# Performance work log

Measured on AMD Instinct MI355X. Metric: run time of the kernel, lower is better.

Reference implementation:

```python
import jax, jax.numpy as jnp
import numpy as np

D_MODEL = 1024
NUM_HEADS = 16
HEAD_DIM = D_MODEL // NUM_HEADS  # 64
ROPE_BASE = 10000.0


def _rope_tables(n_pos, dim):
    # 1D rotary tables for `dim` channels (rotate-half convention).
    inv_freq = 1.0 / (ROPE_BASE ** (jnp.arange(0, dim, 2, dtype=jnp.float32) / dim))
    ang = jnp.arange(n_pos, dtype=jnp.float32)[:, None] * inv_freq[None, :]  # (P, dim/2)
    cos = jnp.concatenate([jnp.cos(ang), jnp.cos(ang)], axis=-1)  # (P, dim)
    sin = jnp.concatenate([jnp.sin(ang), jnp.sin(ang)], axis=-1)
    return cos, sin


def _rotate_half(v):
    v1, v2 = jnp.split(v, 2, axis=-1)
    return jnp.concatenate([-v2, v1], axis=-1)


def rope_2d(x, H, W):
    # x: (N, H, W, nh, hd). First half of hd rotated by row index, second by col index.
    d_half = HEAD_DIM // 2
    x_h, x_w = x[..., :d_half], x[..., d_half:]
    cos_h, sin_h = _rope_tables(H, d_half)  # (H, d_half)
    cos_w, sin_w = _rope_tables(W, d_half)  # (W, d_half)
    cos_h = cos_h[None, :, None, None, :]
    sin_h = sin_h[None, :, None, None, :]
    cos_w = cos_w[None, None, :, None, :]
    sin_w = sin_w[None, None, :, None, :]
    x_h = x_h * cos_h + _rotate_half(x_h) * sin_h
    x_w = x_w * cos_w + _rotate_half(x_w) * sin_w
    return jnp.concatenate([x_h, x_w], axis=-1)


def setup_inputs() -> dict:
    key = jax.random.key(0)
    k_x, k_qkv, k_p, k_b = jax.random.split(key, 4)
    B, T, H, W = 4, 32, 16, 16
    x = jax.random.normal(k_x, (B, T, H, W, D_MODEL), dtype=jnp.float32)
    w_qkv = jax.random.normal(k_qkv, (D_MODEL, 3 * D_MODEL), dtype=jnp.float32) * 0.02
    w_proj = jax.random.normal(k_p, (D_MODEL, D_MODEL), dtype=jnp.float32) * 0.02
    b_proj = jax.random.normal(k_b, (D_MODEL,), dtype=jnp.float32) * 0.02
    return {"x": x, "w_qkv": w_qkv, "w_proj": w_proj, "b_proj": b_proj}


def reference(x, w_qkv, w_proj, b_proj):
    B, T, H, W, C = x.shape
    N, S = B * T, H * W
    scale = HEAD_DIM ** -0.5
    xf = x.reshape(N, S, C)
    qkv = xf @ w_qkv  # (N, S, 3C)  [qkv_bias=False]
    q, k, v = jnp.split(qkv, 3, axis=-1)
    q = q.reshape(N, H, W, NUM_HEADS, HEAD_DIM)
    k = k.reshape(N, H, W, NUM_HEADS, HEAD_DIM)
    v = v.reshape(N, S, NUM_HEADS, HEAD_DIM)
    q = rope_2d(q, H, W).reshape(N, S, NUM_HEADS, HEAD_DIM)
    k = rope_2d(k, H, W).reshape(N, S, NUM_HEADS, HEAD_DIM)
    attn = jnp.einsum('nshd,nthd->nhst', q, k) * scale  # (N, nh, S, S)
    attn = jax.nn.softmax(attn, axis=-1)  # attn_drop=0.0
    out = jnp.einsum('nhst,nthd->nshd', attn, v).reshape(N, S, C)
    out = out @ w_proj + b_proj
    return out.reshape(B, T, H, W, C)
```

## Files before the change

### kernel.cpp

```cpp
#include <hip/hip_runtime.h>
#include <hip/hip_bf16.h>
#include <stdint.h>

typedef __attribute__((ext_vector_type(8))) short bf16x8;
typedef __attribute__((ext_vector_type(4))) float f32x4;
typedef __attribute__((ext_vector_type(4))) unsigned short ushort4_t;

__device__ __forceinline__ unsigned short f2bf(float f) {
  union { float f; unsigned int i; } x; x.f = f;
  return (unsigned short)((x.i + 0x7fffu + ((x.i >> 16) & 1u)) >> 16);
}

__device__ __forceinline__ void gl_lds16(const void* g, void* l) {
  __builtin_amdgcn_global_load_lds(
      (const __attribute__((address_space(1))) unsigned int*)(uintptr_t)g,
      (__attribute__((address_space(3))) unsigned int*)(uint32_t)(uintptr_t)l,
      16, 0, 0);
}

__device__ __forceinline__ void bar() {
  asm volatile("" ::: "memory");
  __builtin_amdgcn_s_barrier();
  asm volatile("" ::: "memory");
}

__constant__ float INVF[16] = {
  1.0f,   0.56234132519f,  0.31622776601f,  0.17782794100f,
  0.1f,   0.056234132519f, 0.031622776601f, 0.017782794100f,
  0.01f,  0.0056234132519f,0.0031622776601f,0.0017782794100f,
  0.001f, 0.00056234132519f,0.00031622776601f,0.00017782794100f
};

__global__ __launch_bounds__(256) void k_conv_x(const float4* __restrict__ src,
                                                ushort4_t* __restrict__ dst, int n4) {
  int i = blockIdx.x * 256 + threadIdx.x;
  if (i < n4) {
    float4 v = src[i];
    ushort4_t r = { f2bf(v.x), f2bf(v.y), f2bf(v.z), f2bf(v.w) };
    dst[i] = r;
  }
}

__global__ __launch_bounds__(256) void k_transpose_bf16(const float* __restrict__ src,
                                                        unsigned short* __restrict__ dst,
                                                        int R, int C) {
  __shared__ unsigned short tile[64][65];
  const int bj = blockIdx.x, bi = blockIdx.y;
  const int t = threadIdx.x, lr = t >> 6, lc = t & 63;
  #pragma unroll
  for (int i = 0; i < 16; i++) {
    int r = i * 4 + lr;
    tile[r][lc] = f2bf(src[(size_t)(bi * 64 + r) * C + bj * 64 + lc]);
  }
  __syncthreads();
  #pragma unroll
  for (int i = 0; i < 16; i++) {
    int r = i * 4 + lr;
    dst[(size_t)(bj * 64 + r) * R + bi * 64 + lc] = tile[lc][r];
  }
}


#define LDA(dst, base, hm)                                                      \
  do {                                                                          \
    _Pragma("unroll") for (int t_ = 0; t_ < 4; t_++) {                          \
      dst[0][t_] = *(const bf16x8*)&base[(wm * 128 + (hm) * 64 + t_ * 16 + cl) * 64 + cf0]; \
      dst[1][t_] = *(const bf16x8*)&base[(wm * 128 + (hm) * 64 + t_ * 16 + cl) * 64 + cf1]; \
    }                                                                           \
  } while (0)

#define LDB(dst, base, hn)                                                      \
  do {                                                                          \
    _Pragma("unroll") for (int u_ = 0; u_ < 2; u_++) {                          \
      dst[0][u_] = *(const bf16x8*)&base[(wn * 64 + (hn) * 32 + u_ * 16 + cl) * 64 + cf0]; \
      dst[1][u_] = *(const bf16x8*)&base[(wn * 64 + (hn) * 32 + u_ * 16 + cl) * 64 + cf1]; \
    }                                                                           \
  } while (0)

#define MFMA_Q(hm, hn, AFR, BVR)                                                \
  do {                                                                          \
    __builtin_amdgcn_s_setprio(1);                                              \
    _Pragma("unroll") for (int kc_ = 0; kc_ < 2; kc_++)                         \
      _Pragma("unroll") for (int mt_ = 0; mt_ < 4; mt_++)                       \
        _Pragma("unroll") for (int u_ = 0; u_ < 2; u_++)                        \
          acc[(hm) * 4 + mt_][(hn) * 2 + u_] =                                  \
              __builtin_amdgcn_mfma_f32_16x16x32_bf16(                          \
                  AFR[kc_][mt_], BVR[kc_][u_],                                  \
                  acc[(hm) * 4 + mt_][(hn) * 2 + u_], 0, 0, 0);                 \
    __builtin_amdgcn_s_setprio(0);                                              \
  } while (0)

#define STAGE_A(tile_, half_)                                                   \
  do {                                                                          \
    const int so_ = ((tile_) & 1) * 16384;                                      \
    const int ko_ = (tile_) * 64;                                               \
    gl_lds16(aP[(half_) * 2] + ko_,     &As[so_ + ((half_) * 2) * 4096 + ldsW]);     \
    gl_lds16(aP[(half_) * 2 + 1] + ko_, &As[so_ + ((half_) * 2 + 1) * 4096 + ldsW]); \
  } while (0)

#define STAGE_B(tile_, half_)                                                   \
  do {                                                                          \
    const int so_ = ((tile_) & 1) * 16384;                                      \
    const int ko_ = (tile_) * 64;                                               \
    gl_lds16(bP[(half_) * 2] + ko_,     &Bs[so_ + ((half_) * 2) * 4096 + ldsW]);     \
    gl_lds16(bP[(half_) * 2 + 1] + ko_, &Bs[so_ + ((half_) * 2 + 1) * 4096 + ldsW]); \
  } while (0)

#define LGKM0() asm volatile("s_waitcnt lgkmcnt(0)" ::: "memory")
#define VMC(n)  asm volatile("s_waitcnt vmcnt(" #n ")" ::: "memory")

template<int F32OUT, int ROPE>
__global__ __launch_bounds__(512, 2) void k_gemm_bt(
    const unsigned short* __restrict__ A, const unsigned short* __restrict__ B,
    unsigned short* __restrict__ Cb, float* __restrict__ Cf,
    const float* __restrict__ bias, int M, int N, int K) {
  __shared__ __align__(16) unsigned short As[2 * 256 * 64];
  __shared__ __align__(16) unsigned short Bs[2 * 256 * 64];
  const int tid = threadIdx.x;
  const int lane = tid & 63, wid = tid >> 6;
  const int cl = lane & 15, gr = lane >> 4;
  const int wm = wid >> 2, wn = wid & 3;
  const int l8 = lane >> 3, l7 = lane & 7;

  const int gx = gridDim.x;
  const int nwg = gx * gridDim.y;
  const int fb = blockIdx.y * gx + blockIdx.x;
  const int q = nwg >> 3;
  const int nid = (fb & 7) * q + (fb >> 3);
  const int bx = nid % gx, by = nid / gx;
  const int mBase = by * 256, nBase = bx * 256;

  const int KT = K >> 6;
  const int ldsW = (wid * 8) * 64;
  const int cf0 = ((0 * 4 + gr) ^ (cl & 7)) * 8;
  const int cf1 = ((1 * 4 + gr) ^ (cl & 7)) * 8;

  const unsigned short* aP[4];
  const unsigned short* bP[4];
  #pragma unroll
  for (int i = 0; i < 4; i++) {
    aP[i] = A + (size_t)(mBase + i * 64 + wid * 8 + l8) * K + (l7 ^ l8) * 8;
    bP[i] = B + (size_t)(nBase + i * 64 + wid * 8 + l8) * K + (l7 ^ l8) * 8;
  }

  const f32x4 zero4 = {0.f, 0.f, 0.f, 0.f};
  f32x4 acc[8][4];
  #pragma unroll
  for (int a = 0; a < 8; a++)
    #pragma unroll
    for (int b = 0; b < 4; b++) acc[a][b] = zero4;

  STAGE_A(0, 0); STAGE_A(0, 1); STAGE_B(0, 0); STAGE_B(0, 1);
  STAGE_B(1, 0); STAGE_B(1, 1);
  VMC(4);
  bar();

  bf16x8 af[2][4], bva[2][2], bvb[2][2];

  for (int c = 0; c < KT; c += 2) {
    const unsigned short* a0 = As;
    const unsigned short* b0 = Bs;
    const unsigned short* a1 = As + 16384;
    const unsigned short* b1 = Bs + 16384;
    const int c2 = c + 2, c3 = c + 3;

    LDA(af, a0, 0); LDB(bva, b0, 0);
    STAGE_A(c + 1, 0);
    asm volatile("s_waitcnt lgkmcnt(8)" ::: "memory");
    bar(); LGKM0();
    MFMA_Q(0, 0, af, bva);
    bar();
    LDB(bvb, b0, 1);
    STAGE_A(c + 1, 1);
    bar(); LGKM0();
    MFMA_Q(0, 1, af, bvb);
    bar();
    LDA(af, a0, 1);
    if (c2 < KT) STAGE_B(c2, 0);
    bar(); LGKM0();
    MFMA_Q(1, 1, af, bvb);
    bar();
    if (c2 < KT) { STAGE_B(c2, 1); VMC(4); } else { VMC(0); }
    bar();
    MFMA_Q(1, 0, af, bva);
    bar();

    LDA(af, a1, 0); LDB(bva, b1, 0);
    if (c2 < KT) STAGE_A(c2, 0);
    asm volatile("s_waitcnt lgkmcnt(8)" ::: "memory");
    bar(); LGKM0();
    MFMA_Q(0, 0, af, bva);
    bar();
    LDB(bvb, b1, 1);
    if (c2 < KT) STAGE_A(c2, 1);
    bar(); LGKM0();
    MFMA_Q(0, 1, af, bvb);
    bar();
    LDA(af, a1, 1);
    if (c3 < KT) STAGE_B(c3, 0);
    bar(); LGKM0();
    MFMA_Q(1, 1, af, bvb);
    bar();
    if (c3 < KT)      { STAGE_B(c3, 1); VMC(4); }
    else if (c2 < KT) { VMC(0); }
    bar();
    MFMA_Q(1, 0, af, bva);
    if (c2 < KT) bar();
  }

  if (ROPE && nBase < 2048) {
    const float f2 = INVF[cl];
    #pragma unroll
    for (int amt = 0; amt < 8; amt++)
      #pragma unroll
      for (int r = 0; r < 4; r++) {
        const int sp = (mBase + wm * 128 + amt * 16 + gr * 4 + r) & 255;
        float sh, ch, sw, cw;
        __sincosf((float)(sp >> 4) * f2, &sh, &ch);
        __sincosf((float)(sp & 15) * f2, &sw, &cw);
        const float a = acc[amt][0][r], b = acc[amt][1][r];
        const float cc = acc[amt][2][r], d = acc[amt][3][r];
        acc[amt][0][r] = a * ch - b * sh;
        acc[amt][1][r] = b * ch + a * sh;
        acc[amt][2][r] = cc * cw - d * sw;
        acc[amt][3][r] = d * cw + cc * sw;
      }
  }

  #pragma unroll
  for (int amt = 0; amt < 8; amt++)
    #pragma unroll
    for (int nt = 0; nt < 4; nt++)
      #pragma unroll
      for (int r = 0; r < 4; r++) {
        const int row = mBase + wm * 128 + amt * 16 + gr * 4 + r;
        const int col = nBase + wn * 64 + nt * 16 + cl;
        const float v = acc[amt][nt][r];
        if (F32OUT) Cf[(size_t)row * N + col] = v + bias[col];
        else        Cb[(size_t)row * N + col] = f2bf(v);
      }
}

__global__ __launch_bounds__(256, 3) void k_attn(const unsigned short* __restrict__ qkv,
                                                 unsigned short* __restrict__ attn_out) {
  __shared__ __align__(16) unsigned short Qp[4][64 * 64];
  __shared__ __align__(16) unsigned short Kt[64 * 64];
  __shared__ __align__(16) unsigned short Vt[64 * 64];
  const int blk = blockIdx.x;
  const int n = blk >> 4, h = blk & 15;
  const int tid = threadIdx.x;
  const int lane = tid & 63, wid = tid >> 6;
  const int cl = lane & 15, gr = lane >> 4;
  const int l8 = lane >> 3, l7 = lane & 7;
  const unsigned short* qbase = qkv + (size_t)n * 256 * 3072 + h * 64;
  const unsigned short* kbase = qbase + 1024;
  const unsigned short* vbase = qbase + 2048;

  #pragma unroll
  for (int i = 0; i < 8; i++)
    gl_lds16(qbase + (size_t)(wid * 64 + i * 8 + l8) * 3072 + (l7 ^ l8) * 8,
             &Qp[wid][i * 8 * 64]);
  #pragma unroll
  for (int i = 0; i < 2; i++) {
    const int r0 = (wid * 2 + i) * 8;
    gl_lds16(kbase + (size_t)(r0 + l8) * 3072 + (l7 ^ l8) * 8, &Kt[r0 * 64]);
  }

  unsigned int vr[2][4];
  #pragma unroll
  for (int i = 0; i < 2; i++) {
    const int u = i * 256 + tid;
    const int t0 = u >> 5, d = (u & 31) * 2;
    #pragma unroll
    for (int k = 0; k < 4; k++)
      vr[i][k] = *(const unsigned int*)(vbase + (size_t)(t0 + 16 * k) * 3072 + d);
  }
  __syncthreads();

  bf16x8 qf[4][2];
  #pragma unroll
  for (int mt = 0; mt < 4; mt++)
    #pragma unroll
    for (int kc = 0; kc < 2; kc++)
      qf[mt][kc] = *(const bf16x8*)&Qp[wid][(mt * 16 + cl) * 64 + ((kc * 4 + gr) ^ (cl & 7)) * 8];

  const f32x4 zero4 = {0.f, 0.f, 0.f, 0.f};
  f32x4 o[4][4];
  float lsum[4][4];
  #pragma unroll
  for (int a = 0; a < 4; a++)
    #pragma unroll
    for (int b = 0; b < 4; b++) { o[a][b] = zero4; lsum[a][b] = 0.f; }

  for (int tc = 0; tc < 4; tc++) {
    #pragma unroll
    for (int i = 0; i < 2; i++) {
      const int u = i * 256 + tid;
      const int t0 = u >> 5, d = (u & 31) * 2;
      const unsigned int r0 = vr[i][0], r1 = vr[i][1], r2 = vr[i][2], r3 = vr[i][3];
      uint2 lo, hi;
      lo.x = (r0 & 0xffffu) | (r1 << 16);
      lo.y = (r2 & 0xffffu) | (r3 << 16);
      hi.x = (r0 >> 16) | (r1 & 0xffff0000u);
      hi.y = (r2 >> 16) | (r3 & 0xffff0000u);
      *(uint2*)&Vt[d * 64 + ((t0 >> 1) ^ (d & 7)) * 8 + (t0 & 1) * 4] = lo;
      const int d1 = d + 1;
      *(uint2*)&Vt[d1 * 64 + ((t0 >> 1) ^ (d1 & 7)) * 8 + (t0 & 1) * 4] = hi;
    }
    if (tc < 3) {
      #pragma unroll
      for (int i = 0; i < 2; i++) {
        const int u = i * 256 + tid;
        const int t0 = u >> 5, d = (u & 31) * 2;
        #pragma unroll
        for (int k = 0; k < 4; k++)
          vr[i][k] = *(const unsigned int*)(vbase + (size_t)((tc + 1) * 64 + t0 + 16 * k) * 3072 + d);
      }
    }

    #pragma unroll
    for (int mt = 0; mt < 4; mt++) {
      f32x4 sacc[4] = {zero4, zero4, zero4, zero4};
      #pragma unroll
      for (int kc = 0; kc < 2; kc++)
        #pragma unroll
        for (int nt = 0; nt < 4; nt++) {
          const bf16x8 kf = *(const bf16x8*)&Kt[(nt * 16 + cl) * 64 + ((kc * 4 + gr) ^ (cl & 7)) * 8];
          sacc[nt] = __builtin_amdgcn_mfma_f32_16x16x32_bf16(qf[mt][kc], kf, sacc[nt], 0, 0, 0);
        }
      #pragma unroll
      for (int r = 0; r < 4; r++) {
        const float p0 = __expf(sacc[0][r] * 0.125f);
        const float p1 = __expf(sacc[1][r] * 0.125f);
        const float p2 = __expf(sacc[2][r] * 0.125f);
        const float p3 = __expf(sacc[3][r] * 0.125f);
        lsum[mt][r] += (p0 + p1) + (p2 + p3);
        float2 f01; f01.x = p0; f01.y = p1;
        float2 f23; f23.x = p2; f23.y = p3;
        __hip_bfloat162 b01 = __float22bfloat162_rn(f01);
        __hip_bfloat162 b23 = __float22bfloat162_rn(f23);
        union { __hip_bfloat162 h; unsigned int u; } c0, c1;
        c0.h = b01; c1.h = b23;
        uint2 w; w.x = c0.u; w.y = c1.u;
        const int m = mt * 16 + gr * 4 + r;
        *(uint2*)&Qp[wid][m * 64 + ((cl >> 1) ^ (m & 7)) * 8 + (cl & 1) * 4] = w;
      }
    }
    __syncthreads();

    if (tc < 3) {
      #pragma unroll
      for (int i = 0; i < 2; i++) {
        const int r0 = (wid * 2 + i) * 8;
        gl_lds16(kbase + (size_t)((tc + 1) * 64 + r0 + l8) * 3072 + (l7 ^ l8) * 8, &Kt[r0 * 64]);
      }
    }

    #pragma unroll
    for (int kc = 0; kc < 2; kc++) {
      bf16x8 vf[4], pf[4];
      #pragma unroll
      for (int dt = 0; dt < 4; dt++)
        vf[dt] = *(const bf16x8*)&Vt[(dt * 16 + cl) * 64 + ((kc * 4 + gr) ^ (cl & 7)) * 8];
      #pragma unroll
      for (int mt = 0; mt < 4; mt++)
        pf[mt] = *(const bf16x8*)&Qp[wid][(mt * 16 + cl) * 64 + ((kc * 4 + gr) ^ (cl & 7)) * 8];
      #pragma unroll
      for (int mt = 0; mt < 4; mt++)
        #pragma unroll
        for (int dt = 0; dt < 4; dt++)
          o[mt][dt] = __builtin_amdgcn_mfma_f32_16x16x32_bf16(pf[mt], vf[dt], o[mt][dt], 0, 0, 0);
    }
    __syncthreads();
  }

  #pragma unroll
  for (int mt = 0; mt < 4; mt++)
    #pragma unroll
    for (int r = 0; r < 4; r++) {
      float l = lsum[mt][r];
      l += __shfl_xor(l, 1);
      l += __shfl_xor(l, 2);
      l += __shfl_xor(l, 4);
      l += __shfl_xor(l, 8);
      const float inv = 1.0f / l;
      const int srow = wid * 64 + mt * 16 + gr * 4 + r;
      #pragma unroll
      for (int dt = 0; dt < 4; dt++)
        attn_out[(size_t)(n * 256 + srow) * 1024 + h * 64 + dt * 16 + cl] =
            f2bf(o[mt][dt][r] * inv);
    }
}

extern "C" void kernel_launch(void* const* d_in, const int* in_sizes, int n_in,
                              void* d_out, int out_size, void* d_ws, size_t ws_size,
                              hipStream_t stream) {
  const float* x      = (const float*)d_in[0];
  const float* w_qkv  = (const float*)d_in[1];
  const float* w_proj = (const float*)d_in[2];
  const float* b_proj = (const float*)d_in[3];
  float* out = (float*)d_out;
  char* ws = (char*)d_ws;

  unsigned short* x_bf    = (unsigned short*)ws;
  unsigned short* wqkvT   = (unsigned short*)(ws + 67108864);
  unsigned short* wprojT  = (unsigned short*)(ws + 73400320);
  unsigned short* qkvb    = (unsigned short*)(ws + 75497472);
  unsigned short* attn_bf = x_bf;

  k_conv_x<<<32768, 256, 0, stream>>>((const float4*)x, (ushort4_t*)x_bf, 8388608);
  k_transpose_bf16<<<dim3(48, 16), 256, 0, stream>>>(w_qkv, wqkvT, 1024, 3072);
  k_transpose_bf16<<<dim3(16, 16), 256, 0, stream>>>(w_proj, wprojT, 1024, 1024);

  k_gemm_bt<0, 1><<<dim3(12, 128), 512, 0, stream>>>(x_bf, wqkvT, qkvb, nullptr, nullptr,
                                                     32768, 3072, 1024);
  k_attn<<<2048, 256, 0, stream>>>(qkvb, attn_bf);

  k_gemm_bt<1, 0><<<dim3(4, 128), 512, 0, stream>>>(attn_bf, wprojT, nullptr, out, b_proj,
                                                    32768, 1024, 1024);
}
```

Measured before the change: 640.8 us.

## Replace ping-pong barrier schedule with simple double-buffered K loop

Rewrites the GEMM main loop from a two-tile, barrier-heavy interleaved schedule into a single-tile-per-iteration double-buffered loop. All global-to-LDS loads for the next tile are issued up front, all LDS fragment reads are issued before the MFMAs with graded lgkmcnt waits, and a single vmcnt(0)+barrier closes each iteration. This removes many workgroup barriers and uses extra registers for a second A fragment set. The trade-off is a full vmcnt(0) stall at the end of each iteration, so global latency may be less hidden than before.

```diff
diff --git a/kernel.cpp b/kernel.cpp
--- a/kernel.cpp
+++ b/kernel.cpp
@@ -106,8 +106,7 @@
     gl_lds16(bP[(half_) * 2 + 1] + ko_, &Bs[so_ + ((half_) * 2 + 1) * 4096 + ldsW]); \
   } while (0)
 
-#define LGKM0() asm volatile("s_waitcnt lgkmcnt(0)" ::: "memory")
-#define VMC(n)  asm volatile("s_waitcnt vmcnt(" #n ")" ::: "memory")
+#define SBAR() __builtin_amdgcn_sched_barrier(0)
 
 template<int F32OUT, int ROPE>
 __global__ __launch_bounds__(512, 2) void k_gemm_bt(
@@ -151,61 +150,44 @@
     for (int b = 0; b < 4; b++) acc[a][b] = zero4;
 
   STAGE_A(0, 0); STAGE_A(0, 1); STAGE_B(0, 0); STAGE_B(0, 1);
-  STAGE_B(1, 0); STAGE_B(1, 1);
-  VMC(4);
+  asm volatile("s_waitcnt vmcnt(0)" ::: "memory");
   bar();
 
-  bf16x8 af[2][4], bva[2][2], bvb[2][2];
-
-  for (int c = 0; c < KT; c += 2) {
-    const unsigned short* a0 = As;
-    const unsigned short* b0 = Bs;
-    const unsigned short* a1 = As + 16384;
-    const unsigned short* b1 = Bs + 16384;
-    const int c2 = c + 2, c3 = c + 3;
-
-    LDA(af, a0, 0); LDB(bva, b0, 0);
-    STAGE_A(c + 1, 0);
+  bf16x8 af0[2][4], af1[2][4], bva[2][2], bvb[2][2];
+
+  for (int c = 0; c < KT; ++c) {
+    const int s = c & 1;
+    const unsigned short* as_ = As + s * 16384;
+    const unsigned short* bs_ = Bs + s * 16384;
+
+    if (c + 1 < KT) {
+      STAGE_A(c + 1, 0); STAGE_A(c + 1, 1);
+      STAGE_B(c + 1, 0); STAGE_B(c + 1, 1);
+    }
+
+    LDA(af0, as_, 0);
+    LDB(bva, bs_, 0);
+    SBAR();
+    LDB(bvb, bs_, 1);
+    SBAR();
+    LDA(af1, as_, 1);
+    SBAR();
+
+    asm volatile("s_waitcnt lgkmcnt(12)" ::: "memory");
+    SBAR();
+    MFMA_Q(0, 0, af0, bva);
     asm volatile("s_waitcnt lgkmcnt(8)" ::: "memory");
-    bar(); LGKM0();
-    MFMA_Q(0, 0, af, bva);
-    bar();
-    LDB(bvb, b0, 1);
-    STAGE_A(c + 1, 1);
-    bar(); LGKM0();
-    MFMA_Q(0, 1, af, bvb);
-    bar();
-    LDA(af, a0, 1);
-    if (c2 < KT) STAGE_B(c2, 0);
-    bar(); LGKM0();
-    MFMA_Q(1, 1, af, bvb);
-    bar();
-    if (c2 < KT) { STAGE_B(c2, 1); VMC(4); } else { VMC(0); }
-    bar();
-    MFMA_Q(1, 0, af, bva);
-    bar();
-
-    LDA(af, a1, 0); LDB(bva, b1, 0);
-    if (c2 < KT) STAGE_A(c2, 0);
-    asm volatile("s_waitcnt lgkmcnt(8)" ::: "memory");
-    bar(); LGKM0();
-    MFMA_Q(0, 0, af, bva);
-    bar();
-    LDB(bvb, b1, 1);
-    if (c2 < KT) STAGE_A(c2, 1);
-    bar(); LGKM0();
-    MFMA_Q(0, 1, af, bvb);
-    bar();
-    LDA(af, a1, 1);
-    if (c3 < KT) STAGE_B(c3, 0);
-    bar(); LGKM0();
-    MFMA_Q(1, 1, af, bvb);
-    bar();
-    if (c3 < KT)      { STAGE_B(c3, 1); VMC(4); }
-    else if (c2 < KT) { VMC(0); }
-    bar();
-    MFMA_Q(1, 0, af, bva);
-    if (c2 < KT) bar();
+    SBAR();
+    MFMA_Q(0, 1, af0, bvb);
+    asm volatile("s_waitcnt lgkmcnt(0)" ::: "memory");
+    SBAR();
+    MFMA_Q(1, 1, af1, bvb);
+    MFMA_Q(1, 0, af1, bva);
+
+    if (c + 1 < KT) {
+      asm volatile("s_waitcnt vmcnt(0)" ::: "memory");
+      bar();
+    }
   }
 
   if (ROPE && nBase < 2048) {
```

Result: no change. 648.1 us (+1.1%).
